# Optimization experiments

Hardware: AMD Instinct MI355X
Metric: run time of the kernel (lower is better)

The kernel has to match this reference:

```python
import jax, jax.numpy as jnp
import numpy as np

STAGE_NUM = 3
EPS = 1e-6
BN_EPS = 1e-5


def setup_inputs() -> dict:
    key = jax.random.key(0)
    ks = jax.random.split(key, 6)
    b, c, h, w, k = 16, 512, 64, 64, 64
    x = jax.random.normal(ks[0], (b, c, h, w), dtype=jnp.float32)
    conv1_w = jax.random.normal(ks[1], (c, c), dtype=jnp.float32) * np.sqrt(2.0 / c)
    conv1_b = jax.random.normal(ks[2], (c,), dtype=jnp.float32) * 0.01
    mu = jax.random.normal(ks[3], (c, k), dtype=jnp.float32) * np.sqrt(2.0 / k)
    mu = mu / (EPS + jnp.linalg.norm(mu, axis=0, keepdims=True))
    conv2_w = jax.random.normal(ks[4], (c, c), dtype=jnp.float32) * np.sqrt(2.0 / c)
    bn_gamma = jnp.ones((c,), dtype=jnp.float32)
    bn_beta = jnp.zeros((c,), dtype=jnp.float32)
    bn_mean = jnp.zeros((c,), dtype=jnp.float32)
    bn_var = jnp.ones((c,), dtype=jnp.float32)
    return {"x": x, "conv1_w": conv1_w, "conv1_b": conv1_b, "mu": mu,
            "conv2_w": conv2_w, "bn_gamma": bn_gamma, "bn_beta": bn_beta,
            "bn_mean": bn_mean, "bn_var": bn_var}


def _l2norm(a, axis):
    return a / (EPS + jnp.linalg.norm(a, axis=axis, keepdims=True))


def reference(x, conv1_w, conv1_b, mu, conv2_w, bn_gamma, bn_beta, bn_mean, bn_var):
    b, c, h, w = x.shape
    n = h * w
    # conv1: 1x1 conv with bias == per-pixel matmul
    x = jnp.einsum('oc,bchw->bohw', conv1_w, x) + conv1_b[None, :, None, None]
    xf = x.reshape(b, c, n)             # (b, c, n)
    x_t = xf.transpose(0, 2, 1)         # (b, n, c)
    m = mu                              # (c, k), broadcast on first iter
    z = None
    for _ in range(STAGE_NUM):
        z = jax.nn.softmax(jnp.matmul(x_t, m), axis=2)        # (b, n, k)
        z_ = z / (EPS + z.sum(axis=1, keepdims=True))          # column-normalize
        m = jnp.matmul(xf, z_)                                 # (b, c, k)
        m = _l2norm(m, axis=1)
    # EM loop is under torch.no_grad in the original
    m = jax.lax.stop_gradient(m)
    z = jax.lax.stop_gradient(z)
    rec = jnp.matmul(m, z.transpose(0, 2, 1))                  # (b, c, n)
    rec = jax.nn.relu(rec).reshape(b, c, h, w)
    # conv2: 1x1 conv (no bias) + BatchNorm (inference form, running stats)
    out = jnp.einsum('oc,bchw->bohw', conv2_w, rec)
    inv = bn_gamma / jnp.sqrt(bn_var + BN_EPS)
    out = out * inv[None, :, None, None] + (bn_beta - bn_mean * inv)[None, :, None, None]
    return out
```

## Files before the change

kernel.cpp:

```cpp
#include <hip/hip_runtime.h>
#include <stdint.h>

#define BB 16
#define CC 512
#define NN 4096
#define KC 64

typedef unsigned short ushort_t;
typedef __attribute__((ext_vector_type(8))) __bf16 bf16x8;
typedef __attribute__((ext_vector_type(4))) float f32x4;

static __device__ __forceinline__ float bu2f(ushort_t u){
  union{unsigned int i; float f;} v; v.i = ((unsigned int)u)<<16; return v.f;
}
static __device__ __forceinline__ ushort_t f2bu(float f){
  unsigned int x = __float_as_uint(f);
  return (ushort_t)((x + 0x7FFFu + ((x>>16)&1u)) >> 16);
}
static __device__ __forceinline__ ushort_t lo_part(float v, ushort_t hi){
  return f2bu(v - bu2f(hi));
}

#define MFMA16(a,b,c) __builtin_amdgcn_mfma_f32_16x16x32_bf16(a,b,c,0,0,0)

template<int ROWS>
static __device__ __forceinline__ void stage_lds(const ushort_t* __restrict__ g, int ld,
                                                 ushort_t* l, int tid){
  int wid = tid >> 6, lane = tid & 63;
  #pragma unroll
  for (int it = 0; it < ROWS/32; ++it){
    int chunk = it*4 + wid;
    int row = chunk*8 + (lane >> 3);
    int seg = (lane & 7) ^ (row & 7);
    const ushort_t* gp = g + (size_t)row*ld + seg*8;
    ushort_t* lp = l + chunk*512;
    __builtin_amdgcn_global_load_lds(
        (const __attribute__((address_space(1))) void*)gp,
        (__attribute__((address_space(3))) void*)lp, 16, 0, 0);
  }
}
static __device__ __forceinline__ bf16x8 frag_ld(const ushort_t* l, int row, int ko){
  return *(const bf16x8*)(l + row*64 + (ko ^ ((row & 7) << 3)));
}

__global__ __launch_bounds__(256) void k_transpose(const float* __restrict__ x,
    ushort_t* __restrict__ xTh, ushort_t* __restrict__ xTl, int hasLo){
  __shared__ ushort_t th[64][68];
  __shared__ ushort_t tl[64][68];
  int b = blockIdx.z, c0 = blockIdx.y*64, n0 = blockIdx.x*64;
  int r16 = threadIdx.x >> 4;
  int q4  = (threadIdx.x & 15) * 4;
  #pragma unroll
  for (int p = 0; p < 4; ++p){
    int row = r16 + p*16;
    size_t off = ((size_t)b*CC + c0 + row)*NN + n0 + q4;
    float4 v = *(const float4*)(x + off);
    ushort_t h0=f2bu(v.x), h1=f2bu(v.y), h2=f2bu(v.z), h3=f2bu(v.w);
    th[q4+0][row]=h0; th[q4+1][row]=h1; th[q4+2][row]=h2; th[q4+3][row]=h3;
    if (hasLo){
      tl[q4+0][row]=lo_part(v.x,h0); tl[q4+1][row]=lo_part(v.y,h1);
      tl[q4+2][row]=lo_part(v.z,h2); tl[q4+3][row]=lo_part(v.w,h3);
    }
  }
  __syncthreads();
  #pragma unroll
  for (int p = 0; p < 4; ++p){
    int nrow = r16 + p*16;
    size_t off = ((size_t)b*NN + n0 + nrow)*CC + c0 + q4;
    ushort4 v;
    v.x = th[nrow][q4+0]; v.y = th[nrow][q4+1]; v.z = th[nrow][q4+2]; v.w = th[nrow][q4+3];
    *(ushort4*)(xTh + off) = v;
    if (hasLo){
      ushort4 u;
      u.x = tl[nrow][q4+0]; u.y = tl[nrow][q4+1]; u.z = tl[nrow][q4+2]; u.w = tl[nrow][q4+3];
      *(ushort4*)(xTl + off) = u;
    }
  }
}

__global__ __launch_bounds__(256) void k_prep(const float* __restrict__ gamma,
    const float* __restrict__ beta, const float* __restrict__ mean,
    const float* __restrict__ var, const float* __restrict__ b1,
    const float* __restrict__ W1, const float* __restrict__ W2,
    const float* __restrict__ mu,
    float* __restrict__ bnscale, float* __restrict__ bnshift,
    float* __restrict__ b1f,
    ushort_t* __restrict__ W1h, ushort_t* __restrict__ W1l,
    ushort_t* __restrict__ W2h, ushort_t* __restrict__ W2l,
    ushort_t* __restrict__ mTh, ushort_t* __restrict__ mTl){
  int t = blockIdx.x*256 + threadIdx.x;
  if (t < CC){
    float inv = gamma[t] * rsqrtf(var[t] + 1e-5f);
    bnscale[t] = inv;
    bnshift[t] = beta[t] - mean[t]*inv;
    b1f[t] = b1[t];
  }
  if (t < CC*CC){
    float w1 = W1[t], w2 = W2[t];
    ushort_t h1 = f2bu(w1), h2 = f2bu(w2);
    W1h[t] = h1; W1l[t] = lo_part(w1,h1);
    W2h[t] = h2; W2l[t] = lo_part(w2,h2);
  }
  if (t < BB*KC*CC){
    int c = t & (CC-1);
    int k = (t >> 9) & (KC-1);
    float v = mu[(size_t)c*KC + k];
    ushort_t h = f2bu(v);
    mTh[t] = h; mTl[t] = lo_part(v,h);
  }
}

__global__ __launch_bounds__(256) void k_conv1(const ushort_t* __restrict__ W1h,
    const ushort_t* __restrict__ W1l, const float* __restrict__ bias,
    const ushort_t* __restrict__ xTh, const ushort_t* __restrict__ xTl, int hasBl,
    ushort_t* __restrict__ xfh, ushort_t* __restrict__ xfl, int hasxfl,
    ushort_t* __restrict__ xt1h, ushort_t* __restrict__ xt1l, int hasxt1l){
  __shared__ __align__(16) ushort_t sm[4*128*64];
  ushort_t* lAh = sm;
  ushort_t* lAl = sm + 128*64;
  ushort_t* lBh = sm + 2*128*64;
  ushort_t* lBl = sm + 3*128*64;
  int b = blockIdx.z, m0 = blockIdx.y*128, n0 = blockIdx.x*128;
  int tid = threadIdx.x, wid = tid>>6, lane = tid&63, quad = lane>>4, l16 = lane&15;
  int wm = wid>>1, wn = wid&1;
  f32x4 zero4 = {0.f,0.f,0.f,0.f};
  f32x4 acc[4][4];
  #pragma unroll
  for (int i=0;i<4;++i){
    #pragma unroll
    for (int j=0;j<4;++j) acc[i][j] = zero4;
  }
  const ushort_t* Aph = W1h + (size_t)m0*CC;
  const ushort_t* Apl = W1l + (size_t)m0*CC;
  const ushort_t* Bph = xTh + ((size_t)b*NN + n0)*CC;
  const ushort_t* Bpl = hasBl ? xTl + ((size_t)b*NN + n0)*CC : nullptr;
  for (int k0 = 0; k0 < CC; k0 += 64){
    stage_lds<128>(Aph + k0, CC, lAh, tid);
    stage_lds<128>(Apl + k0, CC, lAl, tid);
    stage_lds<128>(Bph + k0, CC, lBh, tid);
    if (hasBl) stage_lds<128>(Bpl + k0, CC, lBl, tid);
    __syncthreads();
    #pragma unroll
    for (int kk = 0; kk < 64; kk += 32){
      bf16x8 ah[4], al[4], bh[4], bl[4];
      #pragma unroll
      for (int f=0; f<4; ++f){
        ah[f] = frag_ld(lAh, wm*64 + f*16 + l16, kk + quad*8);
        al[f] = frag_ld(lAl, wm*64 + f*16 + l16, kk + quad*8);
        bh[f] = frag_ld(lBh, wn*64 + f*16 + l16, kk + quad*8);
      }
      if (hasBl){
        #pragma unroll
        for (int f=0; f<4; ++f) bl[f] = frag_ld(lBl, wn*64 + f*16 + l16, kk + quad*8);
      }
      #pragma unroll
      for (int i=0;i<4;++i){
        #pragma unroll
        for (int j=0;j<4;++j){
          acc[i][j] = MFMA16(ah[i], bh[j], acc[i][j]);
          acc[i][j] = MFMA16(al[i], bh[j], acc[i][j]);
        }
      }
      if (hasBl){
        #pragma unroll
        for (int i=0;i<4;++i){
          #pragma unroll
          for (int j=0;j<4;++j) acc[i][j] = MFMA16(ah[i], bl[j], acc[i][j]);
        }
      }
    }
    __syncthreads();
  }
  ushort_t* ct = sm;
  float vals[4][4][4];
  #pragma unroll
  for (int i=0;i<4;++i){
    #pragma unroll
    for (int r=0;r<4;++r){
      int m = wm*64 + i*16 + quad*4 + r;
      float bv = bias[m0 + m];
      #pragma unroll
      for (int j=0;j<4;++j){
        float v = acc[i][j][r] + bv;
        vals[i][j][r] = v;
        ct[m*132 + (wn*64 + j*16 + l16)] = f2bu(v);
      }
    }
  }
  __syncthreads();
  {
    ushort_t* xfp = xfh + (size_t)b*CC*NN + (size_t)m0*NN + n0;
    #pragma unroll
    for (int i = 0; i < 16; ++i){
      int idx = tid + i*256;
      int m = idx >> 5, j4 = (idx & 31)*4;
      *(ushort4*)(xfp + (size_t)m*NN + j4) = *(ushort4*)(ct + m*132 + j4);
    }
    ushort_t* xtp = xt1h + ((size_t)b*NN + n0)*CC + m0;
    #pragma unroll
    for (int i = 0; i < 16; ++i){
      int idx = tid + i*256;
      int nrow = idx >> 5, c4 = (idx & 31)*4;
      ushort4 v;
      v.x = ct[(c4+0)*132 + nrow]; v.y = ct[(c4+1)*132 + nrow];
      v.z = ct[(c4+2)*132 + nrow]; v.w = ct[(c4+3)*132 + nrow];
      *(ushort4*)(xtp + (size_t)nrow*CC + c4) = v;
    }
  }
  if (hasxfl || hasxt1l){
    __syncthreads();
    #pragma unroll
    for (int i=0;i<4;++i){
      #pragma unroll
      for (int r=0;r<4;++r){
        int m = wm*64 + i*16 + quad*4 + r;
        #pragma unroll
        for (int j=0;j<4;++j){
          float v = vals[i][j][r];
          ct[m*132 + (wn*64 + j*16 + l16)] = lo_part(v, f2bu(v));
        }
      }
    }
    __syncthreads();
    if (hasxfl){
      ushort_t* xfp = xfl + (size_t)b*CC*NN + (size_t)m0*NN + n0;
      #pragma unroll
      for (int i = 0; i < 16; ++i){
        int idx = tid + i*256;
        int m = idx >> 5, j4 = (idx & 31)*4;
        *(ushort4*)(xfp + (size_t)m*NN + j4) = *(ushort4*)(ct + m*132 + j4);
      }
    }
    if (hasxt1l){
      ushort_t* xtp = xt1l + ((size_t)b*NN + n0)*CC + m0;
      #pragma unroll
      for (int i = 0; i < 16; ++i){
        int idx = tid + i*256;
        int nrow = idx >> 5, c4 = (idx & 31)*4;
        ushort4 v;
        v.x = ct[(c4+0)*132 + nrow]; v.y = ct[(c4+1)*132 + nrow];
        v.z = ct[(c4+2)*132 + nrow]; v.w = ct[(c4+3)*132 + nrow];
        *(ushort4*)(xtp + (size_t)nrow*CC + c4) = v;
      }
    }
  }
}

__global__ __launch_bounds__(256) void k_logits(const ushort_t* __restrict__ xt1h,
    const ushort_t* __restrict__ xt1l, int hasAl,
    const ushort_t* __restrict__ mTh, const ushort_t* __restrict__ mTl,
    ushort_t* __restrict__ zh, ushort_t* __restrict__ zl,
    ushort_t* __restrict__ zTh, ushort_t* __restrict__ zTl,
    float* __restrict__ colsum){
  __shared__ __align__(16) ushort_t sm[2*128*64 + 2*64*64];
  ushort_t* lAh = sm;
  ushort_t* lAl = sm + 128*64;
  ushort_t* lBh = sm + 2*128*64;
  ushort_t* lBl = sm + 2*128*64 + 64*64;
  int b = blockIdx.y, n0 = blockIdx.x*128;
  int tid = threadIdx.x, wid = tid>>6, lane = tid&63, quad = lane>>4, l16 = lane&15;
  f32x4 zero4 = {0.f,0.f,0.f,0.f};
  f32x4 acc[2][4];
  #pragma unroll
  for (int i=0;i<2;++i){
    #pragma unroll
    for (int j=0;j<4;++j) acc[i][j] = zero4;
  }
  const ushort_t* Aph = xt1h + ((size_t)b*NN + n0)*CC;
  const ushort_t* Apl = hasAl ? xt1l + ((size_t)b*NN + n0)*CC : nullptr;
  const ushort_t* Bph = mTh + (size_t)b*KC*CC;
  const ushort_t* Bpl = mTl + (size_t)b*KC*CC;
  for (int k0 = 0; k0 < CC; k0 += 64){
    stage_lds<128>(Aph + k0, CC, lAh, tid);
    if (hasAl) stage_lds<128>(Apl + k0, CC, lAl, tid);
    stage_lds<64>(Bph + k0, CC, lBh, tid);
    stage_lds<64>(Bpl + k0, CC, lBl, tid);
    __syncthreads();
    #pragma unroll
    for (int kk = 0; kk < 64; kk += 32){
      bf16x8 ah[2], al[2], bh[4], bl[4];
      #pragma unroll
      for (int f=0; f<2; ++f){
        ah[f] = frag_ld(lAh, wid*32 + f*16 + l16, kk + quad*8);
        if (hasAl) al[f] = frag_ld(lAl, wid*32 + f*16 + l16, kk + quad*8);
      }
      #pragma unroll
      for (int f=0; f<4; ++f){
        bh[f] = frag_ld(lBh, f*16 + l16, kk + quad*8);
        bl[f] = frag_ld(lBl, f*16 + l16, kk + quad*8);
      }
      #pragma unroll
      for (int i=0;i<2;++i){
        #pragma unroll
        for (int j=0;j<4;++j){
          acc[i][j] = MFMA16(ah[i], bh[j], acc[i][j]);
          acc[i][j] = MFMA16(ah[i], bl[j], acc[i][j]);
        }
      }
      if (hasAl){
        #pragma unroll
        for (int i=0;i<2;++i){
          #pragma unroll
          for (int j=0;j<4;++j) acc[i][j] = MFMA16(al[i], bh[j], acc[i][j]);
        }
      }
    }
    __syncthreads();
  }
  #pragma unroll
  for (int i=0;i<2;++i){
    #pragma unroll
    for (int r=0;r<4;++r){
      float mx = fmaxf(fmaxf(acc[i][0][r], acc[i][1][r]), fmaxf(acc[i][2][r], acc[i][3][r]));
      mx = fmaxf(mx, __shfl_xor(mx, 1));
      mx = fmaxf(mx, __shfl_xor(mx, 2));
      mx = fmaxf(mx, __shfl_xor(mx, 4));
      mx = fmaxf(mx, __shfl_xor(mx, 8));
      float e0 = __expf(acc[i][0][r]-mx), e1 = __expf(acc[i][1][r]-mx);
      float e2 = __expf(acc[i][2][r]-mx), e3 = __expf(acc[i][3][r]-mx);
      float s = e0+e1+e2+e3;
      s += __shfl_xor(s, 1); s += __shfl_xor(s, 2);
      s += __shfl_xor(s, 4); s += __shfl_xor(s, 8);
      float inv = 1.0f/s;
      acc[i][0][r] = e0*inv; acc[i][1][r] = e1*inv;
      acc[i][2][r] = e2*inv; acc[i][3][r] = e3*inv;
    }
  }
  #pragma unroll
  for (int j=0;j<4;++j){
    float p = 0.f;
    #pragma unroll
    for (int i=0;i<2;++i){
      #pragma unroll
      for (int r=0;r<4;++r) p += acc[i][j][r];
    }
    p += __shfl_xor(p, 16); p += __shfl_xor(p, 32);
    if (lane < 16) atomicAdd(&colsum[b*KC + j*16 + l16], p);
  }
  #pragma unroll
  for (int i=0;i<2;++i){
    int nbase = wid*32 + i*16 + quad*4;
    #pragma unroll
    for (int j=0;j<4;++j){
      int k = j*16 + l16;
      ushort4 vh, vl;
      float a0=acc[i][j][0], a1=acc[i][j][1], a2=acc[i][j][2], a3=acc[i][j][3];
      vh.x=f2bu(a0); vh.y=f2bu(a1); vh.z=f2bu(a2); vh.w=f2bu(a3);
      vl.x=lo_part(a0,vh.x); vl.y=lo_part(a1,vh.y); vl.z=lo_part(a2,vh.z); vl.w=lo_part(a3,vh.w);
      size_t zoff = ((size_t)b*KC + k)*NN + n0 + nbase;
      *(ushort4*)(zTh + zoff) = vh;
      *(ushort4*)(zTl + zoff) = vl;
      const ushort_t* ph = (const ushort_t*)&vh;
      const ushort_t* pl = (const ushort_t*)&vl;
      #pragma unroll
      for (int r=0;r<4;++r){
        size_t o = ((size_t)b*NN + n0 + nbase + r)*KC + k;
        zh[o] = ph[r]; zl[o] = pl[r];
      }
    }
  }
}

__global__ __launch_bounds__(256) void k_mgemm(const ushort_t* __restrict__ xfh,
    const ushort_t* __restrict__ xfl, int hasAl,
    const ushort_t* __restrict__ zTh, const ushort_t* __restrict__ zTl,
    float* __restrict__ m_part){
  __shared__ __align__(16) ushort_t sm[2*128*64 + 2*64*64];
  ushort_t* lAh = sm;
  ushort_t* lAl = sm + 128*64;
  ushort_t* lBh = sm + 2*128*64;
  ushort_t* lBl = sm + 2*128*64 + 64*64;
  int c0 = blockIdx.x*128, slice = blockIdx.y, b = blockIdx.z;
  int tid = threadIdx.x, wid = tid>>6, lane = tid&63, quad = lane>>4, l16 = lane&15;
  f32x4 zero4 = {0.f,0.f,0.f,0.f};
  f32x4 acc[2][4];
  #pragma unroll
  for (int i=0;i<2;++i){
    #pragma unroll
    for (int j=0;j<4;++j) acc[i][j] = zero4;
  }
  const ushort_t* Aph = xfh + ((size_t)b*CC + c0)*NN + slice*512;
  const ushort_t* Apl = hasAl ? xfl + ((size_t)b*CC + c0)*NN + slice*512 : nullptr;
  const ushort_t* Bph = zTh + (size_t)b*KC*NN + slice*512;
  const ushort_t* Bpl = zTl + (size_t)b*KC*NN + slice*512;
  for (int k0 = 0; k0 < 512; k0 += 64){
    stage_lds<128>(Aph + k0, NN, lAh, tid);
    if (hasAl) stage_lds<128>(Apl + k0, NN, lAl, tid);
    stage_lds<64>(Bph + k0, NN, lBh, tid);
    stage_lds<64>(Bpl + k0, NN, lBl, tid);
    __syncthreads();
    #pragma unroll
    for (int kk = 0; kk < 64; kk += 32){
      bf16x8 ah[2], al[2], bh[4], bl[4];
      #pragma unroll
      for (int f=0; f<2; ++f){
        ah[f] = frag_ld(lAh, wid*32 + f*16 + l16, kk + quad*8);
        if (hasAl) al[f] = frag_ld(lAl, wid*32 + f*16 + l16, kk + quad*8);
      }
      #pragma unroll
      for (int f=0; f<4; ++f){
        bh[f] = frag_ld(lBh, f*16 + l16, kk + quad*8);
        bl[f] = frag_ld(lBl, f*16 + l16, kk + quad*8);
      }
      #pragma unroll
      for (int i=0;i<2;++i){
        #pragma unroll
        for (int j=0;j<4;++j){
          acc[i][j] = MFMA16(ah[i], bh[j], acc[i][j]);
          acc[i][j] = MFMA16(ah[i], bl[j], acc[i][j]);
        }
      }
      if (hasAl){
        #pragma unroll
        for (int i=0;i<2;++i){
          #pragma unroll
          for (int j=0;j<4;++j) acc[i][j] = MFMA16(al[i], bh[j], acc[i][j]);
        }
      }
    }
    __syncthreads();
  }
  #pragma unroll
  for (int i=0;i<2;++i){
    int c = c0 + wid*32 + i*16 + quad*4;
    #pragma unroll
    for (int j=0;j<4;++j){
      int k = j*16 + l16;
      *(f32x4*)(m_part + (((size_t)slice*BB + b)*KC + k)*CC + c) = acc[i][j];
    }
  }
}

__global__ __launch_bounds__(256) void k_mnorm(const float* __restrict__ m_part,
    const float* __restrict__ colsum,
    ushort_t* __restrict__ mch, ushort_t* __restrict__ mcl,
    ushort_t* __restrict__ mTh, ushort_t* __restrict__ mTl){
  int k = blockIdx.x, b = blockIdx.y, t = threadIdx.x;
  float v0 = 0.f, v1 = 0.f;
  #pragma unroll
  for (int s = 0; s < 8; ++s){
    const float* p = m_part + (((size_t)s*BB + b)*KC + k)*CC;
    v0 += p[t]; v1 += p[t+256];
  }
  float sk = 1.0f/(1e-6f + colsum[b*KC + k]);
  v0 *= sk; v1 *= sk;
  float ss = v0*v0 + v1*v1;
  #pragma unroll
  for (int off = 1; off < 64; off <<= 1) ss += __shfl_xor(ss, off);
  __shared__ float red[4];
  if ((t&63) == 0) red[t>>6] = ss;
  __syncthreads();
  float inv = 1.0f/(1e-6f + sqrtf(red[0]+red[1]+red[2]+red[3]));
  v0 *= inv; v1 *= inv;
  ushort_t h0 = f2bu(v0), h1 = f2bu(v1);
  ushort_t l0 = lo_part(v0,h0), l1 = lo_part(v1,h1);
  size_t to = ((size_t)b*KC + k)*CC + t;
  mTh[to] = h0; mTh[to+256] = h1;
  mTl[to] = l0; mTl[to+256] = l1;
  size_t co = ((size_t)b*CC + t)*KC + k;
  mch[co] = h0; mch[co + (size_t)256*KC] = h1;
  mcl[co] = l0; mcl[co + (size_t)256*KC] = l1;
}

__global__ __launch_bounds__(256) void k_rec(const ushort_t* __restrict__ zh,
    const ushort_t* __restrict__ zl,
    const ushort_t* __restrict__ mch, const ushort_t* __restrict__ mcl,
    ushort_t* __restrict__ recTh, ushort_t* __restrict__ recTl){
  __shared__ __align__(16) ushort_t sm[4*128*64];
  ushort_t* lAh = sm;
  ushort_t* lAl = sm + 128*64;
  ushort_t* lBh = sm + 2*128*64;
  ushort_t* lBl = sm + 3*128*64;
  int n0 = blockIdx.x*128, c0 = blockIdx.y*128, b = blockIdx.z;
  int tid = threadIdx.x, wid = tid>>6, lane = tid&63, quad = lane>>4, l16 = lane&15;
  int wm = wid>>1, wn = wid&1;
  f32x4 zero4 = {0.f,0.f,0.f,0.f};
  f32x4 acc[4][4];
  #pragma unroll
  for (int i=0;i<4;++i){
    #pragma unroll
    for (int j=0;j<4;++j) acc[i][j] = zero4;
  }
  stage_lds<128>(zh + ((size_t)b*NN + n0)*KC, KC, lAh, tid);
  stage_lds<128>(zl + ((size_t)b*NN + n0)*KC, KC, lAl, tid);
  stage_lds<128>(mch + ((size_t)b*CC + c0)*KC, KC, lBh, tid);
  stage_lds<128>(mcl + ((size_t)b*CC + c0)*KC, KC, lBl, tid);
  __syncthreads();
  #pragma unroll
  for (int kk = 0; kk < 64; kk += 32){
    bf16x8 ah[4], al[4], bh[4], bl[4];
    #pragma unroll
    for (int f=0; f<4; ++f){
      ah[f] = frag_ld(lAh, wm*64 + f*16 + l16, kk + quad*8);
      al[f] = frag_ld(lAl, wm*64 + f*16 + l16, kk + quad*8);
      bh[f] = frag_ld(lBh, wn*64 + f*16 + l16, kk + quad*8);
      bl[f] = frag_ld(lBl, wn*64 + f*16 + l16, kk + quad*8);
    }
    #pragma unroll
    for (int i=0;i<4;++i){
      #pragma unroll
      for (int j=0;j<4;++j){
        acc[i][j] = MFMA16(ah[i], bh[j], acc[i][j]);
        acc[i][j] = MFMA16(ah[i], bl[j], acc[i][j]);
        acc[i][j] = MFMA16(al[i], bh[j], acc[i][j]);
      }
    }
  }
  __syncthreads();
  ushort_t* ct = sm;
  #pragma unroll
  for (int i=0;i<4;++i){
    #pragma unroll
    for (int r=0;r<4;++r){
      int m = wm*64 + i*16 + quad*4 + r;
      #pragma unroll
      for (int j=0;j<4;++j)
        ct[m*132 + (wn*64 + j*16 + l16)] = f2bu(fmaxf(acc[i][j][r], 0.f));
    }
  }
  __syncthreads();
  {
    ushort_t* rp = recTh + ((size_t)b*NN + n0)*CC + c0;
    #pragma unroll
    for (int i = 0; i < 16; ++i){
      int idx = tid + i*256;
      int m = idx >> 5, j4 = (idx & 31)*4;
      *(ushort4*)(rp + (size_t)m*CC + j4) = *(ushort4*)(ct + m*132 + j4);
    }
  }
  __syncthreads();
  #pragma unroll
  for (int i=0;i<4;++i){
    #pragma unroll
    for (int r=0;r<4;++r){
      int m = wm*64 + i*16 + quad*4 + r;
      #pragma unroll
      for (int j=0;j<4;++j){
        float v = fmaxf(acc[i][j][r], 0.f);
        ct[m*132 + (wn*64 + j*16 + l16)] = lo_part(v, f2bu(v));
      }
    }
  }
  __syncthreads();
  {
    ushort_t* rp = recTl + ((size_t)b*NN + n0)*CC + c0;
    #pragma unroll
    for (int i = 0; i < 16; ++i){
      int idx = tid + i*256;
      int m = idx >> 5, j4 = (idx & 31)*4;
      *(ushort4*)(rp + (size_t)m*CC + j4) = *(ushort4*)(ct + m*132 + j4);
    }
  }
}

__global__ __launch_bounds__(256) void k_conv2(const ushort_t* __restrict__ W2h,
    const ushort_t* __restrict__ W2l,
    const ushort_t* __restrict__ recTh, const ushort_t* __restrict__ recTl,
    const float* __restrict__ bnscale, const float* __restrict__ bnshift,
    float* __restrict__ out){
  __shared__ __align__(16) ushort_t sm[4*128*64];
  ushort_t* lAh = sm;
  ushort_t* lAl = sm + 128*64;
  ushort_t* lBh = sm + 2*128*64;
  ushort_t* lBl = sm + 3*128*64;
  int b = blockIdx.z, m0 = blockIdx.y*128, n0 = blockIdx.x*128;
  int tid = threadIdx.x, wid = tid>>6, lane = tid&63, quad = lane>>4, l16 = lane&15;
  int wm = wid>>1, wn = wid&1;
  f32x4 zero4 = {0.f,0.f,0.f,0.f};
  f32x4 acc[4][4];
  #pragma unroll
  for (int i=0;i<4;++i){
    #pragma unroll
    for (int j=0;j<4;++j) acc[i][j] = zero4;
  }
  const ushort_t* Aph = W2h + (size_t)m0*CC;
  const ushort_t* Apl = W2l + (size_t)m0*CC;
  const ushort_t* Bph = recTh + ((size_t)b*NN + n0)*CC;
  const ushort_t* Bpl = recTl + ((size_t)b*NN + n0)*CC;
  for (int k0 = 0; k0 < CC; k0 += 64){
    stage_lds<128>(Aph + k0, CC, lAh, tid);
    stage_lds<128>(Apl + k0, CC, lAl, tid);
    stage_lds<128>(Bph + k0, CC, lBh, tid);
    stage_lds<128>(Bpl + k0, CC, lBl, tid);
    __syncthreads();
    #pragma unroll
    for (int kk = 0; kk < 64; kk += 32){
      bf16x8 ah[4], al[4], bh[4], bl[4];
      #pragma unroll
      for (int f=0; f<4; ++f){
        ah[f] = frag_ld(lAh, wm*64 + f*16 + l16, kk + quad*8);
        al[f] = frag_ld(lAl, wm*64 + f*16 + l16, kk + quad*8);
        bh[f] = frag_ld(lBh, wn*64 + f*16 + l16, kk + quad*8);
        bl[f] = frag_ld(lBl, wn*64 + f*16 + l16, kk + quad*8);
      }
      #pragma unroll
      for (int i=0;i<4;++i){
        #pragma unroll
        for (int j=0;j<4;++j){
          acc[i][j] = MFMA16(ah[i], bh[j], acc[i][j]);
          acc[i][j] = MFMA16(ah[i], bl[j], acc[i][j]);
          acc[i][j] = MFMA16(al[i], bh[j], acc[i][j]);
        }
      }
    }
    __syncthreads();
  }
  size_t base = (size_t)b*CC*NN;
  #pragma unroll
  for (int i=0;i<4;++i){
    #pragma unroll
    for (int r=0;r<4;++r){
      int m = m0 + wm*64 + i*16 + quad*4 + r;
      float sc = bnscale[m], sh = bnshift[m];
      #pragma unroll
      for (int j=0;j<4;++j){
        int nn = n0 + wn*64 + j*16 + l16;
        out[base + (size_t)m*NN + nn] = acc[i][j][r]*sc + sh;
      }
    }
  }
}

extern "C" void kernel_launch(void* const* d_in, const int* in_sizes, int n_in,
                              void* d_out, int out_size, void* d_ws, size_t ws_size,
                              hipStream_t stream) {
  (void)in_sizes; (void)n_in; (void)out_size;
  const float* x     = (const float*)d_in[0];
  const float* W1    = (const float*)d_in[1];
  const float* b1    = (const float*)d_in[2];
  const float* mu    = (const float*)d_in[3];
  const float* W2    = (const float*)d_in[4];
  const float* gamma = (const float*)d_in[5];
  const float* beta  = (const float*)d_in[6];
  const float* mean  = (const float*)d_in[7];
  const float* var   = (const float*)d_in[8];
  float* out = (float*)d_out;

  const size_t big = (size_t)BB*NN*CC*2;
  const size_t zsz = (size_t)BB*NN*KC*2;
  char* w = (char*)d_ws;
  ushort_t* xTh  = (ushort_t*)w;  w += big;
  ushort_t* zh   = xTh;
  ushort_t* zl   = (ushort_t*)((char*)xTh + zsz);
  ushort_t* zTh  = (ushort_t*)((char*)xTh + 2*zsz);
  ushort_t* zTl  = (ushort_t*)((char*)xTh + 3*zsz);
  float*    m_part = (float*)((char*)xTh + 4*zsz);
  ushort_t* xfh  = (ushort_t*)w;  w += big;
  ushort_t* xt1h = (ushort_t*)w;  w += big;
  ushort_t* mTh  = (ushort_t*)w;  w += (size_t)BB*KC*CC*2;
  ushort_t* mTl  = (ushort_t*)w;  w += (size_t)BB*KC*CC*2;
  ushort_t* mch  = (ushort_t*)w;  w += (size_t)BB*KC*CC*2;
  ushort_t* mcl  = (ushort_t*)w;  w += (size_t)BB*KC*CC*2;
  ushort_t* W1h  = (ushort_t*)w;  w += (size_t)CC*CC*2;
  ushort_t* W1l  = (ushort_t*)w;  w += (size_t)CC*CC*2;
  ushort_t* W2h  = (ushort_t*)w;  w += (size_t)CC*CC*2;
  ushort_t* W2l  = (ushort_t*)w;  w += (size_t)CC*CC*2;
  float*    bnscale = (float*)w;  w += 2048;
  float*    bnshift = (float*)w;  w += 2048;
  float*    b1f  = (float*)w;     w += 2048;
  float*    colsum = (float*)w;   w += (size_t)BB*KC*4;
  ushort_t* xTl = nullptr; ushort_t* xt1l = nullptr; ushort_t* xfl = nullptr;
  size_t used = (size_t)(w - (char*)d_ws);
  if (used + big <= ws_size){ xTl  = (ushort_t*)w; w += big; used += big; }
  if (used + big <= ws_size){ xt1l = (ushort_t*)w; w += big; used += big; }
  if (used + big <= ws_size){ xfl  = (ushort_t*)w; w += big; used += big; }
  int hasxTl = xTl != nullptr, hasxt1l = xt1l != nullptr, hasxfl = xfl != nullptr;
  ushort_t* recTh = xt1h;
  ushort_t* recTl = hasxt1l ? xt1l : xfh;

  k_transpose<<<dim3(NN/64, CC/64, BB), 256, 0, stream>>>(x, xTh, xTl, hasxTl);
  k_prep<<<dim3((BB*KC*CC + 255)/256), 256, 0, stream>>>(gamma, beta, mean, var, b1,
      W1, W2, mu, bnscale, bnshift, b1f, W1h, W1l, W2h, W2l, mTh, mTl);
  k_conv1<<<dim3(NN/128, CC/128, BB), 256, 0, stream>>>(W1h, W1l, b1f, xTh, xTl, hasxTl,
      xfh, xfl, hasxfl, xt1h, xt1l, hasxt1l);
  for (int it = 0; it < 3; ++it){
    (void)hipMemsetAsync(colsum, 0, (size_t)BB*KC*4, stream);
    k_logits<<<dim3(NN/128, BB), 256, 0, stream>>>(xt1h, xt1l, hasxt1l, mTh, mTl,
        zh, zl, zTh, zTl, colsum);
    k_mgemm<<<dim3(CC/128, 8, BB), 256, 0, stream>>>(xfh, xfl, hasxfl, zTh, zTl, m_part);
    k_mnorm<<<dim3(KC, BB), 256, 0, stream>>>(m_part, colsum, mch, mcl, mTh, mTl);
  }
  k_rec<<<dim3(NN/128, CC/128, BB), 256, 0, stream>>>(zh, zl, mch, mcl, recTh, recTl);
  k_conv2<<<dim3(NN/128, CC/128, BB), 256, 0, stream>>>(W2h, W2l, recTh, recTl,
      bnscale, bnshift, out);
}
```

Before: 793.6 us.

## Fold conv1 weights into EM logits via W1^T·mu instead of storing transposed conv1 output

Computes logits as x^T·(W1^T m) + b1·m by precomputing a small per-batch projected matrix PT and bias term q each iteration. This removes the transposed conv1 output buffer (xt1h/xt1l) and its transposed writes in conv1. Logits now read the original transposed input directly. It also writes the row-major z only on the final iteration. The cost is extra small GEMM/reduction launches per iteration and some additional rounding from the reassociated product.

```diff
diff --git a/kernel.cpp b/kernel.cpp
--- a/kernel.cpp
+++ b/kernel.cpp
@@ -85,7 +85,7 @@
     const float* __restrict__ mu,
     float* __restrict__ bnscale, float* __restrict__ bnshift,
     float* __restrict__ b1f,
-    ushort_t* __restrict__ W1h, ushort_t* __restrict__ W1l,
+    ushort_t* __restrict__ W1Th, ushort_t* __restrict__ W1Tl,
     ushort_t* __restrict__ W2h, ushort_t* __restrict__ W2l,
     ushort_t* __restrict__ mTh, ushort_t* __restrict__ mTl){
   int t = blockIdx.x*256 + threadIdx.x;
@@ -96,9 +96,10 @@
     b1f[t] = b1[t];
   }
   if (t < CC*CC){
+    int o = t >> 9, c = t & (CC-1);
     float w1 = W1[t], w2 = W2[t];
     ushort_t h1 = f2bu(w1), h2 = f2bu(w2);
-    W1h[t] = h1; W1l[t] = lo_part(w1,h1);
+    W1Th[(size_t)c*CC + o] = h1; W1Tl[(size_t)c*CC + o] = lo_part(w1,h1);
     W2h[t] = h2; W2l[t] = lo_part(w2,h2);
   }
   if (t < BB*KC*CC){
@@ -110,11 +111,10 @@
   }
 }
 
-__global__ __launch_bounds__(256) void k_conv1(const ushort_t* __restrict__ W1h,
-    const ushort_t* __restrict__ W1l, const float* __restrict__ bias,
+__global__ __launch_bounds__(256) void k_conv1(const ushort_t* __restrict__ W1Th,
+    const ushort_t* __restrict__ W1Tl, const float* __restrict__ bias,
     const ushort_t* __restrict__ xTh, const ushort_t* __restrict__ xTl, int hasBl,
-    ushort_t* __restrict__ xfh, ushort_t* __restrict__ xfl, int hasxfl,
-    ushort_t* __restrict__ xt1h, ushort_t* __restrict__ xt1l, int hasxt1l){
+    ushort_t* __restrict__ xfh, ushort_t* __restrict__ xfl, int hasxfl){
   __shared__ __align__(16) ushort_t sm[4*128*64];
   ushort_t* lAh = sm;
   ushort_t* lAl = sm + 128*64;
@@ -130,6 +130,30 @@
     #pragma unroll
     for (int j=0;j<4;++j) acc[i][j] = zero4;
   }
+  (void)W1Th; (void)W1Tl; (void)hasBl; (void)xTl; (void)xTh; (void)bias;
+  (void)xfh; (void)xfl; (void)hasxfl; (void)lAh; (void)lAl; (void)lBh; (void)lBl;
+  (void)b; (void)m0; (void)n0; (void)wm; (void)wn; (void)quad; (void)l16;
+}
+
+__global__ __launch_bounds__(256) void k_conv1r(const ushort_t* __restrict__ W1h,
+    const ushort_t* __restrict__ W1l, const float* __restrict__ bias,
+    const ushort_t* __restrict__ xTh, const ushort_t* __restrict__ xTl, int hasBl,
+    ushort_t* __restrict__ xfh, ushort_t* __restrict__ xfl, int hasxfl){
+  __shared__ __align__(16) ushort_t sm[4*128*64];
+  ushort_t* lAh = sm;
+  ushort_t* lAl = sm + 128*64;
+  ushort_t* lBh = sm + 2*128*64;
+  ushort_t* lBl = sm + 3*128*64;
+  int b = blockIdx.z, m0 = blockIdx.y*128, n0 = blockIdx.x*128;
+  int tid = threadIdx.x, wid = tid>>6, lane = tid&63, quad = lane>>4, l16 = lane&15;
+  int wm = wid>>1, wn = wid&1;
+  f32x4 zero4 = {0.f,0.f,0.f,0.f};
+  f32x4 acc[4][4];
+  #pragma unroll
+  for (int i=0;i<4;++i){
+    #pragma unroll
+    for (int j=0;j<4;++j) acc[i][j] = zero4;
+  }
   const ushort_t* Aph = W1h + (size_t)m0*CC;
   const ushort_t* Apl = W1l + (size_t)m0*CC;
   const ushort_t* Bph = xTh + ((size_t)b*NN + n0)*CC;
@@ -196,18 +220,8 @@
       int m = idx >> 5, j4 = (idx & 31)*4;
       *(ushort4*)(xfp + (size_t)m*NN + j4) = *(ushort4*)(ct + m*132 + j4);
     }
-    ushort_t* xtp = xt1h + ((size_t)b*NN + n0)*CC + m0;
-    #pragma unroll
-    for (int i = 0; i < 16; ++i){
-      int idx = tid + i*256;
-      int nrow = idx >> 5, c4 = (idx & 31)*4;
-      ushort4 v;
-      v.x = ct[(c4+0)*132 + nrow]; v.y = ct[(c4+1)*132 + nrow];
-      v.z = ct[(c4+2)*132 + nrow]; v.w = ct[(c4+3)*132 + nrow];
-      *(ushort4*)(xtp + (size_t)nrow*CC + c4) = v;
-    }
-  }
-  if (hasxfl || hasxt1l){
+  }
+  if (hasxfl){
     __syncthreads();
     #pragma unroll
     for (int i=0;i<4;++i){
@@ -222,34 +236,107 @@
       }
     }
     __syncthreads();
-    if (hasxfl){
-      ushort_t* xfp = xfl + (size_t)b*CC*NN + (size_t)m0*NN + n0;
-      #pragma unroll
-      for (int i = 0; i < 16; ++i){
-        int idx = tid + i*256;
-        int m = idx >> 5, j4 = (idx & 31)*4;
-        *(ushort4*)(xfp + (size_t)m*NN + j4) = *(ushort4*)(ct + m*132 + j4);
-      }
-    }
-    if (hasxt1l){
-      ushort_t* xtp = xt1l + ((size_t)b*NN + n0)*CC + m0;
-      #pragma unroll
-      for (int i = 0; i < 16; ++i){
-        int idx = tid + i*256;
-        int nrow = idx >> 5, c4 = (idx & 31)*4;
-        ushort4 v;
-        v.x = ct[(c4+0)*132 + nrow]; v.y = ct[(c4+1)*132 + nrow];
-        v.z = ct[(c4+2)*132 + nrow]; v.w = ct[(c4+3)*132 + nrow];
-        *(ushort4*)(xtp + (size_t)nrow*CC + c4) = v;
-      }
-    }
-  }
-}
-
-__global__ __launch_bounds__(256) void k_logits(const ushort_t* __restrict__ xt1h,
-    const ushort_t* __restrict__ xt1l, int hasAl,
+    ushort_t* xfp = xfl + (size_t)b*CC*NN + (size_t)m0*NN + n0;
+    #pragma unroll
+    for (int i = 0; i < 16; ++i){
+      int idx = tid + i*256;
+      int m = idx >> 5, j4 = (idx & 31)*4;
+      *(ushort4*)(xfp + (size_t)m*NN + j4) = *(ushort4*)(ct + m*132 + j4);
+    }
+  }
+}
+
+__global__ __launch_bounds__(256) void k_q(const float* __restrict__ b1f,
     const ushort_t* __restrict__ mTh, const ushort_t* __restrict__ mTl,
-    ushort_t* __restrict__ zh, ushort_t* __restrict__ zl,
+    float* __restrict__ qout){
+  int b = blockIdx.x, t = threadIdx.x;
+  int k = t & 63, seg = t >> 6;
+  const ushort_t* mh = mTh + (size_t)b*KC*CC + (size_t)k*CC;
+  const ushort_t* ml = mTl + (size_t)b*KC*CC + (size_t)k*CC;
+  float s = 0.f;
+  #pragma unroll 4
+  for (int o = seg*128; o < seg*128 + 128; ++o)
+    s += b1f[o]*(bu2f(mh[o]) + bu2f(ml[o]));
+  __shared__ float red[256];
+  red[t] = s; __syncthreads();
+  if (seg == 0) qout[b*KC + k] = red[k] + red[64+k] + red[128+k] + red[192+k];
+}
+
+__global__ __launch_bounds__(256) void k_wm(const ushort_t* __restrict__ W1Th,
+    const ushort_t* __restrict__ W1Tl,
+    const ushort_t* __restrict__ mTh, const ushort_t* __restrict__ mTl,
+    ushort_t* __restrict__ PTh, ushort_t* __restrict__ PTl){
+  __shared__ __align__(16) ushort_t sm[2*128*64 + 2*64*64];
+  ushort_t* lAh = sm;
+  ushort_t* lAl = sm + 128*64;
+  ushort_t* lBh = sm + 2*128*64;
+  ushort_t* lBl = sm + 2*128*64 + 64*64;
+  int b = blockIdx.y, c0 = blockIdx.x*128;
+  int tid = threadIdx.x, wid = tid>>6, lane = tid&63, quad = lane>>4, l16 = lane&15;
+  f32x4 zero4 = {0.f,0.f,0.f,0.f};
+  f32x4 acc[2][4];
+  #pragma unroll
+  for (int i=0;i<2;++i){
+    #pragma unroll
+    for (int j=0;j<4;++j) acc[i][j] = zero4;
+  }
+  const ushort_t* Aph = W1Th + (size_t)c0*CC;
+  const ushort_t* Apl = W1Tl + (size_t)c0*CC;
+  const ushort_t* Bph = mTh + (size_t)b*KC*CC;
+  const ushort_t* Bpl = mTl + (size_t)b*KC*CC;
+  for (int k0 = 0; k0 < CC; k0 += 64){
+    stage_lds<128>(Aph + k0, CC, lAh, tid);
+    stage_lds<128>(Apl + k0, CC, lAl, tid);
+    stage_lds<64>(Bph + k0, CC, lBh, tid);
+    stage_lds<64>(Bpl + k0, CC, lBl, tid);
+    __syncthreads();
+    #pragma unroll
+    for (int kk = 0; kk < 64; kk += 32){
+      bf16x8 ah[2], al[2], bh[4], bl[4];
+      #pragma unroll
+      for (int f=0; f<2; ++f){
+        ah[f] = frag_ld(lAh, wid*32 + f*16 + l16, kk + quad*8);
+        al[f] = frag_ld(lAl, wid*32 + f*16 + l16, kk + quad*8);
+      }
+      #pragma unroll
+      for (int f=0; f<4; ++f){
+        bh[f] = frag_ld(lBh, f*16 + l16, kk + quad*8);
+        bl[f] = frag_ld(lBl, f*16 + l16, kk + quad*8);
+      }
+      #pragma unroll
+      for (int i=0;i<2;++i){
+        #pragma unroll
+        for (int j=0;j<4;++j){
+          acc[i][j] = MFMA16(ah[i], bh[j], acc[i][j]);
+          acc[i][j] = MFMA16(ah[i], bl[j], acc[i][j]);
+          acc[i][j] = MFMA16(al[i], bh[j], acc[i][j]);
+        }
+      }
+    }
+    __syncthreads();
+  }
+  #pragma unroll
+  for (int i=0;i<2;++i){
+    int cbase = c0 + wid*32 + i*16 + quad*4;
+    #pragma unroll
+    for (int j=0;j<4;++j){
+      int k = j*16 + l16;
+      ushort4 vh, vl;
+      float a0=acc[i][j][0], a1=acc[i][j][1], a2=acc[i][j][2], a3=acc[i][j][3];
+      vh.x=f2bu(a0); vh.y=f2bu(a1); vh.z=f2bu(a2); vh.w=f2bu(a3);
+      vl.x=lo_part(a0,vh.x); vl.y=lo_part(a1,vh.y); vl.z=lo_part(a2,vh.z); vl.w=lo_part(a3,vh.w);
+      size_t off = ((size_t)b*KC + k)*CC + cbase;
+      *(ushort4*)(PTh + off) = vh;
+      *(ushort4*)(PTl + off) = vl;
+    }
+  }
+}
+
+__global__ __launch_bounds__(256) void k_logits(const ushort_t* __restrict__ xTh,
+    const ushort_t* __restrict__ xTl, int hasAl,
+    const ushort_t* __restrict__ PTh, const ushort_t* __restrict__ PTl,
+    const float* __restrict__ q,
+    ushort_t* __restrict__ zh, ushort_t* __restrict__ zl, int writeZ,
     ushort_t* __restrict__ zTh, ushort_t* __restrict__ zTl,
     float* __restrict__ colsum){
   __shared__ __align__(16) ushort_t sm[2*128*64 + 2*64*64];
@@ -266,10 +353,10 @@
     #pragma unroll
     for (int j=0;j<4;++j) acc[i][j] = zero4;
   }
-  const ushort_t* Aph = xt1h + ((size_t)b*NN + n0)*CC;
-  const ushort_t* Apl = hasAl ? xt1l + ((size_t)b*NN + n0)*CC : nullptr;
-  const ushort_t* Bph = mTh + (size_t)b*KC*CC;
-  const ushort_t* Bpl = mTl + (size_t)b*KC*CC;
+  const ushort_t* Aph = xTh + ((size_t)b*NN + n0)*CC;
+  const ushort_t* Apl = hasAl ? xTl + ((size_t)b*NN + n0)*CC : nullptr;
+  const ushort_t* Bph = PTh + (size_t)b*KC*CC;
+  const ushort_t* Bpl = PTl + (size_t)b*KC*CC;
   for (int k0 = 0; k0 < CC; k0 += 64){
     stage_lds<128>(Aph + k0, CC, lAh, tid);
     if (hasAl) stage_lds<128>(Apl + k0, CC, lAl, tid);
@@ -307,10 +394,15 @@
     }
     __syncthreads();
   }
+  float qv[4];
+  #pragma unroll
+  for (int j=0;j<4;++j) qv[j] = q[b*KC + j*16 + l16];
   #pragma unroll
   for (int i=0;i<2;++i){
     #pragma unroll
     for (int r=0;r<4;++r){
+      #pragma unroll
+      for (int j=0;j<4;++j) acc[i][j][r] += qv[j];
       float mx = fmaxf(fmaxf(acc[i][0][r], acc[i][1][r]), fmaxf(acc[i][2][r], acc[i][3][r]));
       mx = fmaxf(mx, __shfl_xor(mx, 1));
       mx = fmaxf(mx, __shfl_xor(mx, 2));
@@ -350,12 +442,14 @@
       size_t zoff = ((size_t)b*KC + k)*NN + n0 + nbase;
       *(ushort4*)(zTh + zoff) = vh;
       *(ushort4*)(zTl + zoff) = vl;
-      const ushort_t* ph = (const ushort_t*)&vh;
-      const ushort_t* pl = (const ushort_t*)&vl;
-      #pragma unroll
-      for (int r=0;r<4;++r){
-        size_t o = ((size_t)b*NN + n0 + nbase + r)*KC + k;
-        zh[o] = ph[r]; zl[o] = pl[r];
+      if (writeZ){
+        const ushort_t* ph = (const ushort_t*)&vh;
+        const ushort_t* pl = (const ushort_t*)&vl;
+        #pragma unroll
+        for (int r=0;r<4;++r){
+          size_t o = ((size_t)b*NN + n0 + nbase + r)*KC + k;
+          zh[o] = ph[r]; zl[o] = pl[r];
+        }
       }
     }
   }
@@ -621,6 +715,16 @@
   }
 }
 
+__global__ __launch_bounds__(256) void k_prep2(const float* __restrict__ W1,
+    ushort_t* __restrict__ W1h, ushort_t* __restrict__ W1l){
+  int t = blockIdx.x*256 + threadIdx.x;
+  if (t < CC*CC){
+    float w1 = W1[t];
+    ushort_t h1 = f2bu(w1);
+    W1h[t] = h1; W1l[t] = lo_part(w1,h1);
+  }
+}
+
 extern "C" void kernel_launch(void* const* d_in, const int* in_sizes, int n_in,
                               void* d_out, int out_size, void* d_ws, size_t ws_size,
                               hipStream_t stream) {
@@ -638,45 +742,52 @@
 
   const size_t big = (size_t)BB*NN*CC*2;
   const size_t zsz = (size_t)BB*NN*KC*2;
+  const size_t msz = (size_t)BB*KC*CC*2;
   char* w = (char*)d_ws;
   ushort_t* xTh  = (ushort_t*)w;  w += big;
-  ushort_t* zh   = xTh;
-  ushort_t* zl   = (ushort_t*)((char*)xTh + zsz);
-  ushort_t* zTh  = (ushort_t*)((char*)xTh + 2*zsz);
-  ushort_t* zTl  = (ushort_t*)((char*)xTh + 3*zsz);
-  float*    m_part = (float*)((char*)xTh + 4*zsz);
   ushort_t* xfh  = (ushort_t*)w;  w += big;
-  ushort_t* xt1h = (ushort_t*)w;  w += big;
-  ushort_t* mTh  = (ushort_t*)w;  w += (size_t)BB*KC*CC*2;
-  ushort_t* mTl  = (ushort_t*)w;  w += (size_t)BB*KC*CC*2;
-  ushort_t* mch  = (ushort_t*)w;  w += (size_t)BB*KC*CC*2;
-  ushort_t* mcl  = (ushort_t*)w;  w += (size_t)BB*KC*CC*2;
+  ushort_t* zh   = (ushort_t*)w;  w += zsz;
+  ushort_t* zl   = (ushort_t*)w;  w += zsz;
+  ushort_t* zTh  = (ushort_t*)w;  w += zsz;
+  ushort_t* zTl  = (ushort_t*)w;  w += zsz;
+  float*    m_part = (float*)w;   w += (size_t)8*BB*KC*CC*4;
+  ushort_t* mTh  = (ushort_t*)w;  w += msz;
+  ushort_t* mTl  = (ushort_t*)w;  w += msz;
+  ushort_t* mch  = (ushort_t*)w;  w += msz;
+  ushort_t* mcl  = (ushort_t*)w;  w += msz;
+  ushort_t* PTh  = (ushort_t*)w;  w += msz;
+  ushort_t* PTl  = (ushort_t*)w;  w += msz;
   ushort_t* W1h  = (ushort_t*)w;  w += (size_t)CC*CC*2;
   ushort_t* W1l  = (ushort_t*)w;  w += (size_t)CC*CC*2;
+  ushort_t* W1Th = (ushort_t*)w;  w += (size_t)CC*CC*2;
+  ushort_t* W1Tl = (ushort_t*)w;  w += (size_t)CC*CC*2;
   ushort_t* W2h  = (ushort_t*)w;  w += (size_t)CC*CC*2;
   ushort_t* W2l  = (ushort_t*)w;  w += (size_t)CC*CC*2;
   float*    bnscale = (float*)w;  w += 2048;
   float*    bnshift = (float*)w;  w += 2048;
   float*    b1f  = (float*)w;     w += 2048;
   float*    colsum = (float*)w;   w += (size_t)BB*KC*4;
-  ushort_t* xTl = nullptr; ushort_t* xt1l = nullptr; ushort_t* xfl = nullptr;
+  float*    qbuf = (float*)w;     w += (size_t)BB*KC*4;
+  ushort_t* xTl = nullptr; ushort_t* xfl = nullptr;
   size_t used = (size_t)(w - (char*)d_ws);
-  if (used + big <= ws_size){ xTl  = (ushort_t*)w; w += big; used += big; }
-  if (used + big <= ws_size){ xt1l = (ushort_t*)w; w += big; used += big; }
-  if (used + big <= ws_size){ xfl  = (ushort_t*)w; w += big; used += big; }
-  int hasxTl = xTl != nullptr, hasxt1l = xt1l != nullptr, hasxfl = xfl != nullptr;
-  ushort_t* recTh = xt1h;
-  ushort_t* recTl = hasxt1l ? xt1l : xfh;
+  if (used + big <= ws_size){ xTl = (ushort_t*)w; w += big; used += big; }
+  if (used + big <= ws_size){ xfl = (ushort_t*)w; w += big; used += big; }
+  int hasxTl = xTl != nullptr, hasxfl = xfl != nullptr;
+  ushort_t* recTh = xfh;
+  ushort_t* recTl = xTh;
 
   k_transpose<<<dim3(NN/64, CC/64, BB), 256, 0, stream>>>(x, xTh, xTl, hasxTl);
   k_prep<<<dim3((BB*KC*CC + 255)/256), 256, 0, stream>>>(gamma, beta, mean, var, b1,
-      W1, W2, mu, bnscale, bnshift, b1f, W1h, W1l, W2h, W2l, mTh, mTl);
-  k_conv1<<<dim3(NN/128, CC/128, BB), 256, 0, stream>>>(W1h, W1l, b1f, xTh, xTl, hasxTl,
-      xfh, xfl, hasxfl, xt1h, xt1l, hasxt1l);
+      W1, W2, mu, bnscale, bnshift, b1f, W1Th, W1Tl, W2h, W2l, mTh, mTl);
+  k_prep2<<<dim3((CC*CC + 255)/256), 256, 0, stream>>>(W1, W1h, W1l);
+  k_conv1r<<<dim3(NN/128, CC/128, BB), 256, 0, stream>>>(W1h, W1l, b1f, xTh, xTl, hasxTl,
+      xfh, xfl, hasxfl);
   for (int it = 0; it < 3; ++it){
     (void)hipMemsetAsync(colsum, 0, (size_t)BB*KC*4, stream);
-    k_logits<<<dim3(NN/128, BB), 256, 0, stream>>>(xt1h, xt1l, hasxt1l, mTh, mTl,
-        zh, zl, zTh, zTl, colsum);
+    k_q<<<dim3(BB), 256, 0, stream>>>(b1f, mTh, mTl, qbuf);
+    k_wm<<<dim3(CC/128, BB), 256, 0, stream>>>(W1Th, W1Tl, mTh, mTl, PTh, PTl);
+    k_logits<<<dim3(NN/128, BB), 256, 0, stream>>>(xTh, xTl, hasxTl, PTh, PTl, qbuf,
+        zh, zl, (it == 2) ? 1 : 0, zTh, zTl, colsum);
     k_mgemm<<<dim3(CC/128, 8, BB), 256, 0, stream>>>(xfh, xfl, hasxfl, zTh, zTl, m_part);
     k_mnorm<<<dim3(KC, BB), 256, 0, stream>>>(m_part, colsum, mch, mcl, mTh, mTl);
   }
```

Result: slower. 828.2 us (+4.4%).
